# Kernel optimization log

Hardware: AMD Instinct MI355X
Metric: run time of the kernel (lower is better)

Reference implementation:

```python
import jax, jax.numpy as jnp
import numpy as np
from jax import lax

N, D = 65536, 6
NUM_SAMPLES, NUM_GROUPS, EMBED_DIM = 2048, 64, 512
EPS = 1e-5


def farthest_point_sampling(points_xyz, num_samples, key):
    # Sequential FPS via lax.scan: squared-euclidean min-distance update + argmax.
    n = points_xyz.shape[0]
    first = jax.random.randint(key, (), 0, n)
    dists0 = jnp.full((n,), jnp.inf, dtype=points_xyz.dtype)

    def step(carry, _):
        dists, last = carry
        d = jnp.sum((points_xyz - points_xyz[last]) ** 2, axis=-1)  # [n]
        dists = jnp.minimum(dists, d)
        dists = dists.at[last].set(-jnp.inf)  # never re-pick sampled points
        nxt = jnp.argmax(dists)
        return (dists, nxt), nxt

    (_, _), rest = lax.scan(step, (dists0, first), None, length=num_samples - 1)
    return jnp.concatenate([first[None], rest])  # [num_samples]


def bn(x, scale, bias):
    # flax nn.BatchNorm (training stats): normalize over all axes but the last.
    mean = x.mean(axis=(0, 1), keepdims=True)
    var = x.var(axis=(0, 1), keepdims=True)
    return scale * (x - mean) * lax.rsqrt(var + EPS) + bias


def setup_inputs() -> dict:
    key = jax.random.key(0)
    ks = jax.random.split(key, 3)
    points = jax.random.normal(ks[0], (N, D), dtype=jnp.float32)
    W1 = jax.random.normal(ks[1], (2 * D, EMBED_DIM), dtype=jnp.float32) * (1.0 / np.sqrt(2 * D))
    W2 = jax.random.normal(ks[2], (EMBED_DIM, EMBED_DIM), dtype=jnp.float32) * (1.0 / np.sqrt(EMBED_DIM))
    return {
        "points": points,
        "W1": W1, "b1": jnp.zeros((EMBED_DIM,), jnp.float32),
        "scale1": jnp.ones((EMBED_DIM,), jnp.float32), "bias1": jnp.zeros((EMBED_DIM,), jnp.float32),
        "W2": W2, "b2": jnp.zeros((EMBED_DIM,), jnp.float32),
        "scale2": jnp.ones((EMBED_DIM,), jnp.float32), "bias2": jnp.zeros((EMBED_DIM,), jnp.float32),
        "random_key": 1,
    }


def reference(points, W1, b1, scale1, bias1, W2, b2, scale2, bias2, random_key):
    key = jax.random.key(random_key)
    points_xyz = points[:, :3]

    # 1) farthest point sampling -> centroid indices [S]
    sampled_ids = farthest_point_sampling(points_xyz, NUM_SAMPLES, key)
    centroids = points_xyz[sampled_ids]  # [S, 3]

    # 2) KNN via squared-euclidean cdist + approx top-k (matches lax.approx_max_k in source)
    dist = (jnp.sum(centroids ** 2, -1)[:, None]
            + jnp.sum(points_xyz ** 2, -1)[None, :]
            - 2.0 * centroids @ points_xyz.T)  # [S, N]
    groups = lax.approx_max_k(-dist, NUM_GROUPS)[1]  # [S, k] int32

    # 3) gather-group: concat(delta-to-centroid, raw features) -> [S, k, 2D]
    cluster = points[groups]                      # [S, k, D]
    centroid_full = points[sampled_ids]           # [S, D]
    delta = cluster - centroid_full[:, None, :]
    features = jnp.concatenate([delta, cluster], axis=-1)  # [S, k, 2D]

    # 4) Dense + BN + ReLU, twice
    h = jax.nn.relu(bn(features @ W1 + b1, scale1, bias1))  # [S, k, E]
    h = jax.nn.relu(bn(h @ W2 + b2, scale2, bias2))         # [S, k, E]

    # 5) max-pool over the group axis
    return jnp.max(h, axis=1)  # [S, E]
```

## Files before the change

kernel.cpp:

```cpp
#include <hip/hip_runtime.h>
#include <stdint.h>

#define N_PTS 65536
#define DIMS 6
#define NSAMP 2048
#define NGRP 64
#define EMB 512
#define ROWS (NSAMP*NGRP)
#define EPS_BN 1e-5f

#define FIRST_MODE 0

typedef __attribute__((ext_vector_type(8))) short short8;
typedef __attribute__((ext_vector_type(4))) float float4v;

__device__ __forceinline__ unsigned short f2bf(float f) {
  unsigned u = __float_as_uint(f);
  u += 0x7FFFu + ((u >> 16) & 1u);
  return (unsigned short)(u >> 16);
}

__device__ __forceinline__ void tf2x32(unsigned k0, unsigned k1, unsigned &x0, unsigned &x1) {
  unsigned ks[3] = {k0, k1, k0 ^ k1 ^ 0x1BD11BDAu};
  const unsigned R[8] = {13,15,26,6,17,29,16,24};
  x0 += ks[0]; x1 += ks[1];
#pragma unroll
  for (int g = 0; g < 5; ++g) {
#pragma unroll
    for (int j = 0; j < 4; ++j) {
      unsigned r = R[(g & 1) * 4 + j];
      x0 += x1;
      x1 = (x1 << r) | (x1 >> (32 - r));
      x1 ^= x0;
    }
    x0 += ks[(g + 1) % 3];
    x1 += ks[(g + 2) % 3] + (unsigned)(g + 1);
  }
}

__device__ __forceinline__ int compute_first(unsigned seed) {
  unsigned k0 = 0u, k1 = seed;
  unsigned s0, s1;
#if (FIRST_MODE == 0) || (FIRST_MODE == 1)
  { unsigned a0 = 0u, a1 = 1u; tf2x32(k0, k1, a0, a1); s0 = a0; s1 = a1; }
#else
  { unsigned p0 = 0u, p1 = 2u; tf2x32(k0, k1, p0, p1);
    unsigned q0 = 1u, q1 = 3u; tf2x32(k0, k1, q0, q1);
    s0 = p1; s1 = q1; }
#endif
  unsigned b0 = 0u, b1v = 0u; tf2x32(s0, s1, b0, b1v);
#if (FIRST_MODE == 0) || (FIRST_MODE == 3)
  unsigned bits = b0 ^ b1v;
#else
  unsigned bits = b0;
#endif
  return (int)(bits & 0xFFFFu);
}

#define FPSB 16
#define MEGA_BLOCKS 256
#define GB_CAND 512
#define H1B_S 520
#define MEGA_LDS 90112
#define FAST_TRIES 64
#define WARMUP_ITS 4
#define SLOTS ((NSAMP-1)*FPSB)

#define DPPMAX(x, ctrl) do { \
  unsigned _m = (unsigned)__builtin_amdgcn_update_dpp(0, (int)(x), (ctrl), 0xf, 0xf, true); \
  (x) = (x) > _m ? (x) : _m; } while (0)

__device__ __forceinline__ void st_u64_l2(unsigned long long* p, unsigned long long v) {
  asm volatile("global_store_dwordx2 %0, %1, off sc0" :: "v"(p), "v"(v) : "memory");
}
__device__ __forceinline__ unsigned long long ld_u64_l2(const unsigned long long* p) {
  unsigned long long r;
  asm volatile("global_load_dwordx2 %0, %1, off sc0\n\ts_waitcnt vmcnt(0)"
               : "=&v"(r) : "v"(p) : "memory");
  return r;
}

__global__ __launch_bounds__(256) void k_init(const float* __restrict__ pts,
    const float* __restrict__ W2, const int* __restrict__ seed_arr,
    unsigned long long* __restrict__ slot, float* __restrict__ stats,
    float* __restrict__ st2, unsigned short* __restrict__ W2T,
    float4* __restrict__ xyzw, int* __restrict__ sampled) {
  int tid = blockIdx.x * 256 + threadIdx.x;
  if (tid < N_PTS) {
    float x = pts[tid*6], y = pts[tid*6+1], z = pts[tid*6+2];
    float p2 = __fadd_rn(__fadd_rn(__fmul_rn(x,x), __fmul_rn(y,y)), __fmul_rn(z,z));
    xyzw[tid] = make_float4(x, y, z, p2);
  }
#pragma unroll
  for (int i = 0; i < 4; ++i) {
    int e = tid + i*65536;
    int c = e >> 9, k = e & 511;
    W2T[e] = f2bf(W2[k*EMB + c]);
  }
  if (tid < 2*SLOTS) slot[tid] = 0ull;
  if (tid < 4*EMB) stats[tid] = 0.f;
  if (tid < 32*1024) st2[tid] = 0.f;
  if (tid >= 1 && tid < NSAMP) sampled[tid] = -1;
  if (tid == 0) sampled[0] = compute_first((unsigned)seed_arr[0]);
}

__global__ __launch_bounds__(1024) void k_mega(
    const float4* __restrict__ xyzw, const float* __restrict__ pts,
    const float* __restrict__ W1, const float* __restrict__ b1,
    unsigned long long* __restrict__ slot, int* __restrict__ sampled,
    int* __restrict__ groups, float* __restrict__ gsum, float* __restrict__ gss) {
  extern __shared__ __align__(16) char smraw[];
  const int t = threadIdx.x;
  unsigned long long* mirror = slot + SLOTS;
  if ((blockIdx.x & 15) == 0) {
    unsigned long long* blkmax = (unsigned long long*)smraw;
    volatile int* winLDS = (volatile int*)(smraw + 256);
    const int b = blockIdx.x >> 4;
    const int lane = t & 63, wid = t >> 6;
    float px[5], py[5], pz[5], pd[5];
    unsigned nidxu[5];
    if (wid > 0) {
      const int T = b*1024 + t;
#pragma unroll
      for (int i = 0; i < 4; ++i) {
        float4 p = xyzw[T + 16384*i];
        px[i] = p.x; py[i] = p.y; pz[i] = p.z; pd[i] = __builtin_inff();
        nidxu[i] = 0xFFFFFFFFu - (unsigned)(T + 16384*i);
      }
      if (wid <= 4) {
        int e = b*1024 + lane + 16384*(wid - 1);
        float4 p = xyzw[e];
        px[4] = p.x; py[4] = p.y; pz[4] = p.z; pd[4] = __builtin_inff();
        nidxu[4] = 0xFFFFFFFFu - (unsigned)e;
      } else {
        px[4] = 0.f; py[4] = 0.f; pz[4] = 0.f; pd[4] = 0.f;
        nidxu[4] = 0u;
      }
    }
    if (t == 0) { winLDS[0] = -1; winLDS[1] = -1; blkmax[0] = 0ull; blkmax[1] = 0ull; }
    int last = sampled[0] & 0xFFFF;
    bool slowlink = false;
    if (wid == 0) __builtin_amdgcn_s_setprio(3);
    __syncthreads();
    for (int it = 0; it < NSAMP-1; ++it) {
      const int p = it & 1;
      if (wid > 0) {
        float4 cc = xyzw[last];
        unsigned long long best = 1ull;
#pragma unroll
        for (int i = 0; i < 5; ++i) {
          float dx = __fsub_rn(px[i], cc.x);
          float dy = __fsub_rn(py[i], cc.y);
          float dz = __fsub_rn(pz[i], cc.z);
          float d = __fadd_rn(__fadd_rn(__fmul_rn(dx,dx), __fmul_rn(dy,dy)), __fmul_rn(dz,dz));
          pd[i] = fminf(pd[i], d);
          unsigned long long pk = ((unsigned long long)__float_as_uint(pd[i]) << 32)
                                | (unsigned long long)nidxu[i];
          best = best > pk ? best : pk;
        }
        unsigned myd = (unsigned)(best >> 32);
        unsigned r = myd;
        DPPMAX(r, 0x111);
        DPPMAX(r, 0x112);
        DPPMAX(r, 0x114);
        DPPMAX(r, 0x118);
        DPPMAX(r, 0x142);
        DPPMAX(r, 0x143);
        unsigned bd = (unsigned)__builtin_amdgcn_readlane((int)r, 63);
        unsigned long long tie = __ballot(myd == bd);
        unsigned long long wbest;
        if (__popcll(tie) == 1) {
          int wl = (int)__builtin_ctzll(tie);
          unsigned lo = (unsigned)__builtin_amdgcn_readlane((int)(unsigned)best, wl);
          wbest = ((unsigned long long)bd << 32) | (unsigned long long)lo;
        } else {
          wbest = best;
#pragma unroll
          for (int off = 32; off >= 1; off >>= 1) {
            unsigned long long o = __shfl_xor(wbest, off, 64);
            wbest = wbest > o ? wbest : o;
          }
        }
        if (lane == 0) atomicMax(&blkmax[p], wbest);
      }
      __syncthreads();
      if (wid == 0) {
        if (lane == 0) {
          winLDS[1-p] = -1;
          unsigned long long m = blkmax[p];
          blkmax[p] = 0ull;
          st_u64_l2(&mirror[it*FPSB + b], m);
          __hip_atomic_store(&slot[it*FPSB + b], m,
                             __ATOMIC_RELAXED, __HIP_MEMORY_SCOPE_AGENT);
        }
        unsigned long long v = 0ull;
        if (lane < FPSB) {
          unsigned long long* spm = &mirror[it*FPSB + lane];
          unsigned long long* sp  = &slot[it*FPSB + lane];
          if (it >= WARMUP_ITS && !slowlink) {
            int tries = 0;
            do { v = ld_u64_l2(spm); } while (v == 0ull && ++tries < FAST_TRIES);
            if (v == 0ull) slowlink = true;
          }
          if (v == 0ull) {
            do { v = __hip_atomic_load(sp, __ATOMIC_RELAXED, __HIP_MEMORY_SCOPE_AGENT); }
            while (v == 0ull);
          }
        }
        unsigned pd32 = (unsigned)(v >> 32);
        unsigned r2 = pd32;
        DPPMAX(r2, 0x111);
        DPPMAX(r2, 0x112);
        DPPMAX(r2, 0x114);
        DPPMAX(r2, 0x118);
        unsigned bd2 = (unsigned)__builtin_amdgcn_readlane((int)r2, 15);
        unsigned long long tie2 = __ballot((lane < FPSB) && (pd32 == bd2));
        if (__popcll(tie2) == 1) {
          int wl2 = (int)__builtin_ctzll(tie2);
          unsigned lo2 = (unsigned)__builtin_amdgcn_readlane((int)(unsigned)v, wl2);
          v = ((unsigned long long)bd2 << 32) | (unsigned long long)lo2;
        } else {
#pragma unroll
          for (int off = 8; off >= 1; off >>= 1) {
            unsigned long long o = __shfl_xor(v, off, 64);
            v = v > o ? v : o;
          }
          v = __shfl(v, 0, 64);
        }
        int win = (int)(0xFFFFFFFFu - (unsigned)(v & 0xFFFFFFFFull)) & 0xFFFF;
        if (lane == 0) {
          if (b == 0)
            __hip_atomic_store((unsigned*)&sampled[it+1], (unsigned)win,
                               __ATOMIC_RELAXED, __HIP_MEMORY_SCOPE_AGENT);
          winLDS[p] = win;
        }
        last = win;
      } else {
        __builtin_amdgcn_s_setprio(0);
        int w = winLDS[p];
        while (w == -1) { __builtin_amdgcn_s_sleep(1); w = winLDS[p]; }
        __builtin_amdgcn_s_setprio(1);
        last = w;
      }
    }
  } else {
    unsigned* hist  = (unsigned*)smraw;
    unsigned* scan  = (unsigned*)(smraw + 32768);
    unsigned* candK = (unsigned*)(smraw + 36864);
    int*      candI = (int*)(smraw + 38912);
    float*    feat  = (float*)(smraw + 40960);
    float*    cf    = (float*)(smraw + 44032);
    unsigned* ctl   = (unsigned*)(smraw + 44064);
    volatile int* binfo = (volatile int*)(smraw + 44080);
    const int wkr = blockIdx.x - 1 - (blockIdx.x >> 4);
    for (int s = wkr; s < NSAMP; s += MEGA_BLOCKS - FPSB) {
      if (t == 0) {
        unsigned v = __hip_atomic_load((const unsigned*)&sampled[s],
                        __ATOMIC_RELAXED, __HIP_MEMORY_SCOPE_AGENT);
        while (v == 0xFFFFFFFFu) {
          __builtin_amdgcn_s_sleep(64);
          v = __hip_atomic_load((const unsigned*)&sampled[s],
                  __ATOMIC_RELAXED, __HIP_MEMORY_SCOPE_AGENT);
        }
        binfo[2] = (int)(v & 0xFFFFu);
        ctl[0] = 0u; ctl[1] = 0u;
      }
      for (int k = t; k < 8192; k += 1024) hist[k] = 0u;
      __syncthreads();
      const int sid = binfo[2];
      float4 c4 = xyzw[sid];
      const float cx=c4.x, cy=c4.y, cz=c4.z, c2=c4.w;
      for (int i = 0; i < N_PTS/1024; ++i) {
        int j = i*1024 + t;
        float4 p = xyzw[j];
        float dot = __fadd_rn(__fadd_rn(__fmul_rn(cx,p.x),__fmul_rn(cy,p.y)),__fmul_rn(cz,p.z));
        float d = __fsub_rn(__fadd_rn(c2, p.w), __fmul_rn(2.0f, dot));
        unsigned kb = __float_as_uint(d);
        kb ^= ((unsigned)((int)kb >> 31)) | 0x80000000u;
        atomicAdd(&hist[kb >> 19], 1u);
      }
      __syncthreads();
      unsigned ch = 0u;
      for (int k = 0; k < 8; ++k) ch += hist[t*8 + k];
      scan[t] = ch;
      __syncthreads();
      for (int off = 1; off < 1024; off <<= 1) {
        unsigned vv = (t >= off) ? scan[t - off] : 0u;
        __syncthreads();
        scan[t] += vv;
        __syncthreads();
      }
      unsigned inc = scan[t], before = inc - ch;
      if (before < NGRP && inc >= NGRP) {
        unsigned c = before;
        for (int k = 0; k < 8; ++k) {
          unsigned nb = hist[t*8 + k];
          if (c + nb >= NGRP) { binfo[0] = t*8 + k; binfo[1] = (int)c; break; }
          c += nb;
        }
      }
      __syncthreads();
      const unsigned B = (unsigned)binfo[0];
      const int bef = binfo[1];
      for (int i = 0; i < N_PTS/1024; ++i) {
        int j = i*1024 + t;
        float4 p = xyzw[j];
        float dot = __fadd_rn(__fadd_rn(__fmul_rn(cx,p.x),__fmul_rn(cy,p.y)),__fmul_rn(cz,p.z));
        float d = __fsub_rn(__fadd_rn(c2, p.w), __fmul_rn(2.0f, dot));
        unsigned kb = __float_as_uint(d);
        kb ^= ((unsigned)((int)kb >> 31)) | 0x80000000u;
        unsigned bin = kb >> 19;
        if (bin < B) {
          unsigned pos = atomicAdd(&ctl[0], 1u);
          groups[s*NGRP + pos] = j;
        } else if (bin == B) {
          unsigned ci = atomicAdd(&ctl[1], 1u);
          if (ci < GB_CAND) { candK[ci] = kb; candI[ci] = j; }
        }
      }
      __syncthreads();
      int M = ctl[1] < GB_CAND ? (int)ctl[1] : GB_CAND;
      int need = NGRP - bef;
      for (int c = t; c < M; c += 1024) {
        unsigned mk = candK[c]; int mi = candI[c];
        int rank = 0;
        for (int q = 0; q < M; ++q) {
          unsigned qk = candK[q];
          rank += (qk < mk || (qk == mk && candI[q] < mi)) ? 1 : 0;
        }
        if (rank < need) {
          unsigned pos = atomicAdd(&ctl[0], 1u);
          groups[s*NGRP + pos] = candI[c];
        }
      }
      __syncthreads();
      if (t == 0) {
        while (ctl[0] < NGRP) { groups[s*NGRP + ctl[0]] = 0; ctl[0]++; }
      }
      __syncthreads();
      if (t < DIMS) cf[t] = pts[sid*6 + t];
      __syncthreads();
      if (t < NGRP) {
        int g = groups[s*NGRP + t];
#pragma unroll
        for (int k = 0; k < DIMS; ++k) {
          float v = pts[g*6 + k];
          feat[t*12 + k] = v - cf[k];
          feat[t*12 + 6 + k] = v;
        }
      }
      __syncthreads();
      if (t < EMB) {
        float w[12];
#pragma unroll
        for (int k = 0; k < 12; ++k) w[k] = W1[k*EMB + t];
        float b = b1[t];
        float sum = 0.f, ss = 0.f;
        for (int r = 0; r < NGRP; ++r) {
          float y = b;
#pragma unroll
          for (int k = 0; k < 12; ++k) y += feat[r*12+k] * w[k];
          sum += y; ss += y*y;
        }
        atomicAdd(&gsum[t], sum);
        atomicAdd(&gss[t], ss);
      }
      __syncthreads();
    }
  }
}

__global__ __launch_bounds__(EMB) void k_finalize(const float* __restrict__ gsum,
    const float* __restrict__ gss, const float* __restrict__ scale,
    const float* __restrict__ bias, float* __restrict__ ac) {
  int c = threadIdx.x;
  float inv = 1.f / (float)ROWS;
  float mean = gsum[c] * inv;
  float var = gss[c] * inv - mean*mean;
  var = var < 0.f ? 0.f : var;
  float a = scale[c] * rsqrtf(var + EPS_BN);
  ac[c] = a; ac[EMB + c] = bias[c] - mean * a;
}

__global__ __launch_bounds__(EMB) void k_finalize2(const float* __restrict__ st2,
    const float* __restrict__ scale, const float* __restrict__ bias,
    float* __restrict__ ac) {
  int c = threadIdx.x;
  float sum = 0.f, ss = 0.f;
  for (int i = 0; i < 32; ++i) {
    sum += st2[i*1024 + c];
    ss  += st2[i*1024 + 512 + c];
  }
  float inv = 1.f / (float)ROWS;
  float mean = sum * inv;
  float var = ss * inv - mean*mean;
  var = var < 0.f ? 0.f : var;
  float a = scale[c] * rsqrtf(var + EPS_BN);
  ac[c] = a; ac[EMB + c] = bias[c] - mean * a;
}

__global__ __launch_bounds__(512, 4) void k_mlp(const float* __restrict__ pts,
    const int* __restrict__ sampled, const int* __restrict__ groups,
    const float* __restrict__ W1, const float* __restrict__ b1,
    const float* __restrict__ ac1, const unsigned short* __restrict__ W2T,
    const float* __restrict__ b2, const float* __restrict__ scale2,
    float* __restrict__ st2, float* __restrict__ y2sel) {
  const int s = blockIdx.x, t = threadIdx.x;
  extern __shared__ __align__(16) char smc[];
  float* feat = (float*)smc;
  float* cf   = (float*)(smc + 3072);
  unsigned short* h1b = (unsigned short*)(smc + 3104);
  if (t < DIMS) cf[t] = pts[(sampled[s] & 0xFFFF)*6 + t];
  __syncthreads();
  if (t < NGRP) {
    int g = groups[s*NGRP + t];
#pragma unroll
    for (int k = 0; k < DIMS; ++k) {
      float v = pts[g*6 + k];
      feat[t*12+k]   = v - cf[k];
      feat[t*12+6+k] = v;
    }
  }
  __syncthreads();
  {
    float w[12];
#pragma unroll
    for (int k = 0; k < 12; ++k) w[k] = W1[k*EMB + t];
    float b = b1[t], a1 = ac1[t], c1 = ac1[EMB + t];
    for (int r = 0; r < NGRP; ++r) {
      float y = b;
#pragma unroll
      for (int k = 0; k < 12; ++k) y += feat[r*12+k] * w[k];
      float hv = a1*y + c1;
      h1b[r*H1B_S + t] = f2bf(hv > 0.f ? hv : 0.f);
    }
  }
  __syncthreads();
  const int lane = t & 63, w = t >> 6;
  const int quad = lane >> 4, l16 = lane & 15;
  float4v acc[4][4];
#pragma unroll
  for (int nt = 0; nt < 4; ++nt) {
    float bv = b2[(w*4+nt)*16 + l16];
#pragma unroll
    for (int mt = 0; mt < 4; ++mt)
      acc[nt][mt] = (float4v){bv, bv, bv, bv};
  }
  for (int kc = 0; kc < 16; ++kc) {
    const int kb = kc*32 + quad*8;
    short8 af[4];
#pragma unroll
    for (int mt = 0; mt < 4; ++mt)
      af[mt] = *(const short8*)&h1b[(mt*16 + l16)*H1B_S + kb];
#pragma unroll
    for (int nt = 0; nt < 4; ++nt) {
      const int c = (w*4+nt)*16 + l16;
      short8 bf = *(const short8*)&W2T[c*EMB + kb];
#pragma unroll
      for (int mt = 0; mt < 4; ++mt)
        acc[nt][mt] = __builtin_amdgcn_mfma_f32_16x16x32_bf16(af[mt], bf, acc[nt][mt], 0, 0, 0);
    }
  }
#pragma unroll
  for (int nt = 0; nt < 4; ++nt) {
    float sm_ = 0.f, ss_ = 0.f, mx = -__builtin_inff(), mn = __builtin_inff();
#pragma unroll
    for (int mt = 0; mt < 4; ++mt)
#pragma unroll
      for (int i = 0; i < 4; ++i) {
        float v = acc[nt][mt][i];
        sm_ += v; ss_ += v*v;
        mx = fmaxf(mx, v); mn = fminf(mn, v);
      }
#pragma unroll
    for (int off = 16; off <= 32; off <<= 1) {
      sm_ += __shfl_xor(sm_, off, 64);
      ss_ += __shfl_xor(ss_, off, 64);
      mx = fmaxf(mx, __shfl_xor(mx, off, 64));
      mn = fminf(mn, __shfl_xor(mn, off, 64));
    }
    if (quad == 0) {
      int c = (w*4+nt)*16 + l16;
      atomicAdd(&st2[(s & 31)*1024 + c], sm_);
      atomicAdd(&st2[(s & 31)*1024 + 512 + c], ss_);
      y2sel[s*EMB + c] = (scale2[c] >= 0.f) ? mx : mn;
    }
  }
}

__global__ __launch_bounds__(256) void k_out(const float* __restrict__ y2sel,
    const float* __restrict__ ac2, float* __restrict__ out) {
  int i = blockIdx.x*256 + threadIdx.x;
  int c = i & (EMB-1);
  float a = ac2[c], cc = ac2[EMB + c];
  float v = a*y2sel[i] + cc;
  out[i] = v > 0.f ? v : 0.f;
}

extern "C" void kernel_launch(void* const* d_in, const int* in_sizes, int n_in,
                              void* d_out, int out_size, void* d_ws, size_t ws_size,
                              hipStream_t stream) {
  const float* pts    = (const float*)d_in[0];
  const float* W1     = (const float*)d_in[1];
  const float* b1     = (const float*)d_in[2];
  const float* scale1 = (const float*)d_in[3];
  const float* bias1  = (const float*)d_in[4];
  const float* W2     = (const float*)d_in[5];
  const float* b2     = (const float*)d_in[6];
  const float* scale2 = (const float*)d_in[7];
  const float* bias2  = (const float*)d_in[8];
  const int*   seed   = (const int*)d_in[9];
  float* out = (float*)d_out;

  char* ws = (char*)d_ws;
  int*    sampled = (int*)(ws);
  int*    groups  = (int*)(ws + 8192);
  float4* xyzw    = (float4*)(ws + 532480);
  float*  stats   = (float*)(ws + 1581056);
  float* gsum1 = stats, *gss1 = stats + 512;
  float*  ac1     = (float*)(ws + 1589248);
  float*  ac2     = (float*)(ws + 1593344);
  float*  y2sel   = (float*)(ws + 1597440);
  unsigned long long* slot = (unsigned long long*)(ws + 1597440);
  unsigned short* W2T = (unsigned short*)(ws + 5791744);
  float* st2      = (float*)(ws + 6316032);

  k_init<<<256, 256, 0, stream>>>(pts, W2, seed, slot, stats, st2, W2T, xyzw, sampled);
  k_mega<<<MEGA_BLOCKS, 1024, MEGA_LDS, stream>>>(xyzw, pts, W1, b1, slot, sampled,
                                                  groups, gsum1, gss1);
  k_finalize<<<1, EMB, 0, stream>>>(gsum1, gss1, scale1, bias1, ac1);
  size_t mlp_lds = 3104 + (size_t)NGRP * H1B_S * sizeof(unsigned short);
  k_mlp<<<NSAMP, 512, mlp_lds, stream>>>(pts, sampled, groups, W1, b1, ac1,
                                         W2T, b2, scale2, st2, y2sel);
  k_finalize2<<<1, EMB, 0, stream>>>(st2, scale2, bias2, ac2);
  k_out<<<(out_size+255)/256, 256, 0, stream>>>(y2sel, ac2, out);
}
```

Measured before the change: 3.800 ms.

## Carry winner coordinates through FPS cross-block exchange to drop dependent centroid load

The FPS reduction now carries the winning point's xyz alongside the packed distance/index key. It goes through the per-wave LDS slots and the cross-block global exchange, written as four tagged 64-bit words and read back with two dwordx4 loads. This removes the per-iteration dependent global load of xyzw[last] from the critical path. LDS atomicMax is replaced by per-wave slot writes, and slot readiness uses iteration tags instead of zero checks. In exchange, each block stores and polls four times more data per iteration, and the slot buffer grows fourfold.

```diff
diff --git a/kernel.cpp b/kernel.cpp
--- a/kernel.cpp
+++ b/kernel.cpp
@@ -13,6 +13,7 @@
 
 typedef __attribute__((ext_vector_type(8))) short short8;
 typedef __attribute__((ext_vector_type(4))) float float4v;
+typedef __attribute__((ext_vector_type(4))) unsigned uint4v;
 
 __device__ __forceinline__ unsigned short f2bf(float f) {
   unsigned u = __float_as_uint(f);
@@ -64,7 +65,7 @@
 #define MEGA_LDS 90112
 #define FAST_TRIES 64
 #define WARMUP_ITS 4
-#define SLOTS ((NSAMP-1)*FPSB)
+#define SLOTN ((NSAMP-1)*FPSB)
 
 #define DPPMAX(x, ctrl) do { \
   unsigned _m = (unsigned)__builtin_amdgcn_update_dpp(0, (int)(x), (ctrl), 0xf, 0xf, true); \
@@ -73,11 +74,12 @@
 __device__ __forceinline__ void st_u64_l2(unsigned long long* p, unsigned long long v) {
   asm volatile("global_store_dwordx2 %0, %1, off sc0" :: "v"(p), "v"(v) : "memory");
 }
-__device__ __forceinline__ unsigned long long ld_u64_l2(const unsigned long long* p) {
-  unsigned long long r;
-  asm volatile("global_load_dwordx2 %0, %1, off sc0\n\ts_waitcnt vmcnt(0)"
-               : "=&v"(r) : "v"(p) : "memory");
-  return r;
+__device__ __forceinline__ void ld_slots_l2(const unsigned long long* p,
+                                            uint4v &a, uint4v &c) {
+  asm volatile("global_load_dwordx4 %0, %2, off sc0\n\t"
+               "global_load_dwordx4 %1, %2, off offset:16 sc0\n\t"
+               "s_waitcnt vmcnt(0)"
+               : "=&v"(a), "=&v"(c) : "v"(p) : "memory");
 }
 
 __global__ __launch_bounds__(256) void k_init(const float* __restrict__ pts,
@@ -97,7 +99,11 @@
     int c = e >> 9, k = e & 511;
     W2T[e] = f2bf(W2[k*EMB + c]);
   }
-  if (tid < 2*SLOTS) slot[tid] = 0ull;
+#pragma unroll
+  for (int i = 0; i < 4; ++i) {
+    int e = tid + i*65536;
+    if (e < 8*SLOTN) slot[e] = 0ull;
+  }
   if (tid < 4*EMB) stats[tid] = 0.f;
   if (tid < 32*1024) st2[tid] = 0.f;
   if (tid >= 1 && tid < NSAMP) sampled[tid] = -1;
@@ -111,14 +117,19 @@
     int* __restrict__ groups, float* __restrict__ gsum, float* __restrict__ gss) {
   extern __shared__ __align__(16) char smraw[];
   const int t = threadIdx.x;
-  unsigned long long* mirror = slot + SLOTS;
+  unsigned long long* canR = slot;
+  unsigned long long* mirR = slot + 4*SLOTN;
   if ((blockIdx.x & 15) == 0) {
-    unsigned long long* blkmax = (unsigned long long*)smraw;
-    volatile int* winLDS = (volatile int*)(smraw + 256);
+    unsigned long long* wredK = (unsigned long long*)smraw;
+    float* wredX = (float*)(smraw + 256);
+    float* wredY = (float*)(smraw + 384);
+    float* wredZ = (float*)(smraw + 512);
+    volatile int* winB = (volatile int*)(smraw + 640);
     const int b = blockIdx.x >> 4;
     const int lane = t & 63, wid = t >> 6;
     float px[5], py[5], pz[5], pd[5];
     unsigned nidxu[5];
+    float ccx = 0.f, ccy = 0.f, ccz = 0.f;
     if (wid > 0) {
       const int T = b*1024 + t;
 #pragma unroll
@@ -136,27 +147,33 @@
         px[4] = 0.f; py[4] = 0.f; pz[4] = 0.f; pd[4] = 0.f;
         nidxu[4] = 0u;
       }
-    }
-    if (t == 0) { winLDS[0] = -1; winLDS[1] = -1; blkmax[0] = 0ull; blkmax[1] = 0ull; }
-    int last = sampled[0] & 0xFFFF;
+      float4 c0 = xyzw[sampled[0] & 0xFFFF];
+      ccx = c0.x; ccy = c0.y; ccz = c0.z;
+    }
+    if (t < 32) {
+      wredK[t] = 0ull;
+      wredX[t] = 0.f; wredY[t] = 0.f; wredZ[t] = 0.f;
+    }
+    if (t == 0) { winB[0] = 0; winB[4] = 0; }
     bool slowlink = false;
     if (wid == 0) __builtin_amdgcn_s_setprio(3);
     __syncthreads();
     for (int it = 0; it < NSAMP-1; ++it) {
       const int p = it & 1;
+      const unsigned tag = (unsigned)(it + 1);
       if (wid > 0) {
-        float4 cc = xyzw[last];
         unsigned long long best = 1ull;
+        float bx = 0.f, by = 0.f, bz = 0.f;
 #pragma unroll
         for (int i = 0; i < 5; ++i) {
-          float dx = __fsub_rn(px[i], cc.x);
-          float dy = __fsub_rn(py[i], cc.y);
-          float dz = __fsub_rn(pz[i], cc.z);
+          float dx = __fsub_rn(px[i], ccx);
+          float dy = __fsub_rn(py[i], ccy);
+          float dz = __fsub_rn(pz[i], ccz);
           float d = __fadd_rn(__fadd_rn(__fmul_rn(dx,dx), __fmul_rn(dy,dy)), __fmul_rn(dz,dz));
           pd[i] = fminf(pd[i], d);
           unsigned long long pk = ((unsigned long long)__float_as_uint(pd[i]) << 32)
                                 | (unsigned long long)nidxu[i];
-          best = best > pk ? best : pk;
+          if (pk > best) { best = pk; bx = px[i]; by = py[i]; bz = pz[i]; }
         }
         unsigned myd = (unsigned)(best >> 32);
         unsigned r = myd;
@@ -170,8 +187,8 @@
         unsigned long long tie = __ballot(myd == bd);
         unsigned long long wbest;
         if (__popcll(tie) == 1) {
-          int wl = (int)__builtin_ctzll(tie);
-          unsigned lo = (unsigned)__builtin_amdgcn_readlane((int)(unsigned)best, wl);
+          int wl0 = (int)__builtin_ctzll(tie);
+          unsigned lo = (unsigned)__builtin_amdgcn_readlane((int)(unsigned)best, wl0);
           wbest = ((unsigned long long)bd << 32) | (unsigned long long)lo;
         } else {
           wbest = best;
@@ -181,66 +198,140 @@
             wbest = wbest > o ? wbest : o;
           }
         }
-        if (lane == 0) atomicMax(&blkmax[p], wbest);
+        unsigned long long sel = __ballot(best == wbest);
+        int wl = (int)__builtin_ctzll(sel);
+        float wx = __int_as_float(__builtin_amdgcn_readlane(__float_as_int(bx), wl));
+        float wy = __int_as_float(__builtin_amdgcn_readlane(__float_as_int(by), wl));
+        float wz = __int_as_float(__builtin_amdgcn_readlane(__float_as_int(bz), wl));
+        if (lane == 0) {
+          wredK[p*16 + wid] = wbest;
+          wredX[p*16 + wid] = wx;
+          wredY[p*16 + wid] = wy;
+          wredZ[p*16 + wid] = wz;
+        }
       }
       __syncthreads();
       if (wid == 0) {
-        if (lane == 0) {
-          winLDS[1-p] = -1;
-          unsigned long long m = blkmax[p];
-          blkmax[p] = 0ull;
-          st_u64_l2(&mirror[it*FPSB + b], m);
-          __hip_atomic_store(&slot[it*FPSB + b], m,
-                             __ATOMIC_RELAXED, __HIP_MEMORY_SCOPE_AGENT);
-        }
-        unsigned long long v = 0ull;
-        if (lane < FPSB) {
-          unsigned long long* spm = &mirror[it*FPSB + lane];
-          unsigned long long* sp  = &slot[it*FPSB + lane];
-          if (it >= WARMUP_ITS && !slowlink) {
-            int tries = 0;
-            do { v = ld_u64_l2(spm); } while (v == 0ull && ++tries < FAST_TRIES);
-            if (v == 0ull) slowlink = true;
-          }
-          if (v == 0ull) {
-            do { v = __hip_atomic_load(sp, __ATOMIC_RELAXED, __HIP_MEMORY_SCOPE_AGENT); }
-            while (v == 0ull);
-          }
-        }
-        unsigned pd32 = (unsigned)(v >> 32);
-        unsigned r2 = pd32;
-        DPPMAX(r2, 0x111);
-        DPPMAX(r2, 0x112);
-        DPPMAX(r2, 0x114);
-        DPPMAX(r2, 0x118);
+        unsigned long long k16 = 0ull; float kx = 0.f, ky = 0.f, kz = 0.f;
+        if (lane < 16) {
+          k16 = wredK[p*16 + lane];
+          kx = wredX[p*16 + lane]; ky = wredY[p*16 + lane]; kz = wredZ[p*16 + lane];
+        }
+        unsigned d16 = (unsigned)(k16 >> 32);
+        unsigned r2 = d16;
+        DPPMAX(r2, 0x111); DPPMAX(r2, 0x112); DPPMAX(r2, 0x114); DPPMAX(r2, 0x118);
         unsigned bd2 = (unsigned)__builtin_amdgcn_readlane((int)r2, 15);
-        unsigned long long tie2 = __ballot((lane < FPSB) && (pd32 == bd2));
+        unsigned long long tie2 = __ballot((lane < 16) && (d16 == bd2));
+        unsigned long long bk;
         if (__popcll(tie2) == 1) {
           int wl2 = (int)__builtin_ctzll(tie2);
-          unsigned lo2 = (unsigned)__builtin_amdgcn_readlane((int)(unsigned)v, wl2);
-          v = ((unsigned long long)bd2 << 32) | (unsigned long long)lo2;
+          unsigned lo2 = (unsigned)__builtin_amdgcn_readlane((int)(unsigned)k16, wl2);
+          bk = ((unsigned long long)bd2 << 32) | (unsigned long long)lo2;
         } else {
+          unsigned long long tk = (lane < 16) ? k16 : 0ull;
 #pragma unroll
           for (int off = 8; off >= 1; off >>= 1) {
-            unsigned long long o = __shfl_xor(v, off, 64);
-            v = v > o ? v : o;
+            unsigned long long o = __shfl_xor(tk, off, 64);
+            tk = tk > o ? tk : o;
           }
-          v = __shfl(v, 0, 64);
-        }
-        int win = (int)(0xFFFFFFFFu - (unsigned)(v & 0xFFFFFFFFull)) & 0xFFFF;
+          bk = __shfl(tk, 0, 64);
+        }
+        unsigned long long selB = __ballot((lane < 16) && (k16 == bk));
+        int wlB = (int)__builtin_ctzll(selB);
+        unsigned bxu = (unsigned)__builtin_amdgcn_readlane(__float_as_int(kx), wlB);
+        unsigned byu = (unsigned)__builtin_amdgcn_readlane(__float_as_int(ky), wlB);
+        unsigned bzu = (unsigned)__builtin_amdgcn_readlane(__float_as_int(kz), wlB);
+        if (lane == 0) {
+          unsigned lo16 = (unsigned)bk & 0xFFFFu;
+          unsigned lowT = ((tag & 0xFFFFu) << 16) | lo16;
+          unsigned long long w0 = ((bk >> 32) << 32) | (unsigned long long)lowT;
+          unsigned long long w1 = ((unsigned long long)bxu << 32) | (unsigned long long)lowT;
+          unsigned long long w2 = ((unsigned long long)byu << 32) | (unsigned long long)lowT;
+          unsigned long long w3 = ((unsigned long long)bzu << 32) | (unsigned long long)lowT;
+          unsigned long long* mb = &mirR[(unsigned)(it*FPSB + b)*4];
+          st_u64_l2(mb+0, w0); st_u64_l2(mb+1, w1);
+          st_u64_l2(mb+2, w2); st_u64_l2(mb+3, w3);
+          unsigned long long* cb = &canR[(unsigned)(it*FPSB + b)*4];
+          __hip_atomic_store(cb+0, w0, __ATOMIC_RELAXED, __HIP_MEMORY_SCOPE_AGENT);
+          __hip_atomic_store(cb+1, w1, __ATOMIC_RELAXED, __HIP_MEMORY_SCOPE_AGENT);
+          __hip_atomic_store(cb+2, w2, __ATOMIC_RELAXED, __HIP_MEMORY_SCOPE_AGENT);
+          __hip_atomic_store(cb+3, w3, __ATOMIC_RELAXED, __HIP_MEMORY_SCOPE_AGENT);
+        }
+        unsigned long long v0 = 0ull, v1 = 0ull, v2 = 0ull, v3 = 0ull;
+        bool useFast = (it >= WARMUP_ITS) && !slowlink;
+        int tries = 0;
+        for (;;) {
+          bool stale = false, ready = false;
+          if (lane < FPSB) {
+            if (useFast) {
+              uint4v a, c;
+              ld_slots_l2(&mirR[(unsigned)(it*FPSB + lane)*4], a, c);
+              v0 = ((unsigned long long)a[1] << 32) | a[0];
+              v1 = ((unsigned long long)a[3] << 32) | a[2];
+              v2 = ((unsigned long long)c[1] << 32) | c[0];
+              v3 = ((unsigned long long)c[3] << 32) | c[2];
+            } else {
+              const unsigned long long* cb = &canR[(unsigned)(it*FPSB + lane)*4];
+              v0 = __hip_atomic_load(cb+0, __ATOMIC_RELAXED, __HIP_MEMORY_SCOPE_AGENT);
+              v1 = __hip_atomic_load(cb+1, __ATOMIC_RELAXED, __HIP_MEMORY_SCOPE_AGENT);
+              v2 = __hip_atomic_load(cb+2, __ATOMIC_RELAXED, __HIP_MEMORY_SCOPE_AGENT);
+              v3 = __hip_atomic_load(cb+3, __ATOMIC_RELAXED, __HIP_MEMORY_SCOPE_AGENT);
+            }
+            unsigned l0 = (unsigned)v0, l1 = (unsigned)v1;
+            unsigned l2_ = (unsigned)v2, l3 = (unsigned)v3;
+            ready = ((l0 >> 16) == tag) && ((l1 >> 16) == tag) &&
+                    ((l2_ >> 16) == tag) && ((l3 >> 16) == tag);
+            stale = (l0 == 0u) || (l1 == 0u) || (l2_ == 0u) || (l3 == 0u);
+          }
+          if (__ballot(stale) == 0ull) {
+            if (!ready) { v0 = 0ull; v1 = 0ull; v2 = 0ull; v3 = 0ull; }
+            break;
+          }
+          if (useFast && ++tries >= FAST_TRIES) { slowlink = true; useFast = false; }
+        }
+        unsigned pd32 = (unsigned)(v0 >> 32);
+        unsigned r3 = pd32;
+        DPPMAX(r3, 0x111); DPPMAX(r3, 0x112); DPPMAX(r3, 0x114); DPPMAX(r3, 0x118);
+        unsigned bd3 = (unsigned)__builtin_amdgcn_readlane((int)r3, 15);
+        unsigned long long tie3 = __ballot((lane < FPSB) && (pd32 == bd3));
+        unsigned long long g0;
+        if (__popcll(tie3) == 1) {
+          int wl3 = (int)__builtin_ctzll(tie3);
+          unsigned lo3 = (unsigned)__builtin_amdgcn_readlane((int)(unsigned)v0, wl3);
+          g0 = ((unsigned long long)bd3 << 32) | (unsigned long long)lo3;
+        } else {
+          unsigned long long tv = (lane < FPSB) ? v0 : 0ull;
+#pragma unroll
+          for (int off = 8; off >= 1; off >>= 1) {
+            unsigned long long o = __shfl_xor(tv, off, 64);
+            tv = tv > o ? tv : o;
+          }
+          g0 = __shfl(tv, 0, 64);
+        }
+        unsigned long long selG = __ballot((lane < FPSB) && (v0 == g0));
+        int wlG = (selG != 0ull) ? (int)__builtin_ctzll(selG) : 0;
+        unsigned gxu = (unsigned)__builtin_amdgcn_readlane((int)(unsigned)(v1 >> 32), wlG);
+        unsigned gyu = (unsigned)__builtin_amdgcn_readlane((int)(unsigned)(v2 >> 32), wlG);
+        unsigned gzu = (unsigned)__builtin_amdgcn_readlane((int)(unsigned)(v3 >> 32), wlG);
+        int win = (int)(0xFFFFu - ((unsigned)g0 & 0xFFFFu)) & 0xFFFF;
         if (lane == 0) {
           if (b == 0)
             __hip_atomic_store((unsigned*)&sampled[it+1], (unsigned)win,
                                __ATOMIC_RELAXED, __HIP_MEMORY_SCOPE_AGENT);
-          winLDS[p] = win;
-        }
-        last = win;
+          winB[p*4 + 1] = (int)gxu;
+          winB[p*4 + 2] = (int)gyu;
+          winB[p*4 + 3] = (int)gzu;
+          asm volatile("s_waitcnt lgkmcnt(0)" ::: "memory");
+          winB[p*4 + 0] = (int)((tag << 16) | (unsigned)win);
+        }
       } else {
         __builtin_amdgcn_s_setprio(0);
-        int w = winLDS[p];
-        while (w == -1) { __builtin_amdgcn_s_sleep(1); w = winLDS[p]; }
+        int w0l = winB[p*4];
+        while (((unsigned)w0l >> 16) != tag) { __builtin_amdgcn_s_sleep(1); w0l = winB[p*4]; }
         __builtin_amdgcn_s_setprio(1);
-        last = w;
+        ccx = __int_as_float(winB[p*4 + 1]);
+        ccy = __int_as_float(winB[p*4 + 2]);
+        ccz = __int_as_float(winB[p*4 + 3]);
       }
     }
   } else {
```

After: 7.689 ms. 102% more time.
